# Performance work log

Measured on AMD Instinct MI355X. Metric: run time of the kernel, lower is better.

The kernel has to match this reference:

```python
import jax, jax.numpy as jnp
import numpy as np
from jax import lax

SCALE = 4
PATCH = 3
CR = 2
SOFTMAX_FACTOR = 10.0
B, H, W, C = 8, 64, 64, 64
CI = C // CR


def prelu(x, alpha):
    return jnp.where(x >= 0, x, alpha * x)


def conv1x1(x, w, b):
    return jnp.einsum('bhwc,cd->bhwd', x, w) + b


def _same_pad(in_size, k, s):
    out = -(-in_size // s)
    pad = max((out - 1) * s + k - in_size, 0)
    return pad // 2, pad - pad // 2, out


def extract_patches(x, k, s):
    # x: [B,H,W,C] -> [B, outH, outW, k, k, C], SAME zero padding (TF extract_patches)
    b, h, w, c = x.shape
    plh, phh, oh = _same_pad(h, k, s)
    plw, phw, ow = _same_pad(w, k, s)
    xp = jnp.pad(x, ((0, 0), (plh, phh), (plw, phw), (0, 0)))
    rows = (jnp.arange(oh) * s)[:, None] + jnp.arange(k)[None, :]  # [oh,k]
    cols = (jnp.arange(ow) * s)[:, None] + jnp.arange(k)[None, :]  # [ow,k]
    p = xp[:, rows]              # [B, oh, k, Wp, C]
    p = p[:, :, :, cols]         # [B, oh, k, ow, k, C]
    return p.transpose(0, 1, 3, 2, 4, 5)


def setup_inputs() -> dict:
    key = jax.random.key(0)
    ks = jax.random.split(key, 8)
    def glorot(k, shape):
        fan_in, fan_out = shape[0], shape[1]
        std = np.sqrt(2.0 / (fan_in + fan_out))
        return jax.random.normal(k, shape, dtype=jnp.float32) * std
    return {
        'x': jax.random.normal(ks[0], (B, H, W, C), dtype=jnp.float32),
        'theta_w': glorot(ks[1], (C, CI)),
        'theta_b': jnp.zeros((CI,), jnp.float32),
        'theta_alpha': jax.random.uniform(ks[2], (CI,), jnp.float32, 0.0, 0.3),
        'phi_w': glorot(ks[3], (C, CI)),
        'phi_b': jnp.zeros((CI,), jnp.float32),
        'phi_alpha': jax.random.uniform(ks[4], (CI,), jnp.float32, 0.0, 0.3),
        'g_w': glorot(ks[5], (C, C)),
        'g_b': jnp.zeros((C,), jnp.float32),
        'g_alpha': jax.random.uniform(ks[6], (C,), jnp.float32, 0.0, 0.3),
    }


def reference(x, theta_w, theta_b, theta_alpha, phi_w, phi_b, phi_alpha, g_w, g_b, g_alpha):
    b, h, w, c = x.shape
    s, p = SCALE, PATCH
    hs, ws = h // s, w // s
    n = hs * ws
    sp = s * p
    ci = c // CR

    theta = prelu(conv1x1(x, theta_w, theta_b), theta_alpha)                  # [B,H,W,Ci]
    phi_in = jax.image.resize(x, (b, hs, ws, c), method='bilinear', antialias=False)
    phi = prelu(conv1x1(phi_in, phi_w, phi_b), phi_alpha)                     # [B,Hs,Ws,Ci]
    phi_patch = extract_patches(phi, p, 1).reshape(b, n, p, p, ci)            # [B,N,3,3,Ci]
    g = prelu(conv1x1(x, g_w, g_b), g_alpha)                                  # [B,H,W,C]
    g_patch = extract_patches(g, sp, s).reshape(b, n, sp, sp, c)              # [B,N,12,12,C]

    # L2-normalize each phi patch (per patch, over kh,kw,ci)
    norm = jnp.sqrt(jnp.sum(phi_patch * phi_patch, axis=(2, 3, 4), keepdims=True))
    phi_n = phi_patch / jnp.maximum(norm, 1e-6)

    # patch matching == SAME 3x3 correlation of theta with N dynamic filters
    theta_patch = extract_patches(theta, p, 1)                                # [B,H,W,3,3,Ci]
    scores = jnp.einsum('bhwpqc,bnpqc->bhwn', theta_patch, phi_n)             # [B,H,W,N]
    attn = jax.nn.softmax(scores * SOFTMAX_FACTOR, axis=-1)

    # conv2d_transpose with per-sample filters [sp,sp,C,N], stride s, SAME
    pad_lo, pad_hi, _ = _same_pad(s * h, sp, s)  # forward-conv SAME pads (4,4)
    pads = (sp - 1 - pad_lo, sp - 1 - pad_hi)

    def deconv(y_i, g_i):
        # y_i: [H,W,N]; g_i: [N,sp,sp,C]
        ker = g_i.transpose(1, 2, 0, 3)[::-1, ::-1]  # spatially flipped, HWIO (I=N,O=C)
        out = lax.conv_general_dilated(
            y_i[None], ker, window_strides=(1, 1),
            padding=[pads, pads], lhs_dilation=(s, s),
            dimension_numbers=('NHWC', 'HWIO', 'NHWC'))
        return out[0]

    y = jax.vmap(deconv)(attn, g_patch)  # [B, s*H, s*W, C]
    return y / 6.0
```

## Files before the change

### kernel.cpp

```cpp
#include <hip/hip_runtime.h>
#include <math.h>

#define BB 8

typedef __attribute__((ext_vector_type(8))) short short8;
typedef __attribute__((ext_vector_type(4))) float f32x4;

__device__ inline short f2bf(float x) {
  unsigned u = __builtin_bit_cast(unsigned, x);
  u += 0x7fffu + ((u >> 16) & 1u);
  return (short)(u >> 16);
}
__device__ inline float bf2f(short h) {
  unsigned u = ((unsigned)(unsigned short)h) << 16;
  return __builtin_bit_cast(float, u);
}

__device__ inline void gload_lds16(const void* g, void* l) {
  __builtin_amdgcn_global_load_lds(
      (const __attribute__((address_space(1))) void*)g,
      (__attribute__((address_space(3))) void*)l, 16, 0, 0);
}

__device__ inline void ring_px(int p, int& r, int& cc) {
  if (p < 66) { r = 0; cc = p; }
  else if (p < 132) { r = 65; cc = p - 66; }
  else { int q = p - 132; r = 1 + (q >> 1); cc = (q & 1) ? 65 : 0; }
}

__global__ __launch_bounds__(256) void k_pre(const float* __restrict__ x,
                          const float* __restrict__ theta_w, const float* __restrict__ theta_b,
                          const float* __restrict__ theta_alpha,
                          const float* __restrict__ phi_w, const float* __restrict__ phi_b,
                          const float* __restrict__ phi_alpha,
                          const float* __restrict__ g_w, const float* __restrict__ g_b,
                          const float* __restrict__ g_alpha,
                          short* __restrict__ thetaPh, short* __restrict__ thetaPl,
                          short* __restrict__ gOut,
                          short* __restrict__ Bh, short* __restrict__ Bl) {
  __shared__ __align__(16) float spool[14528];
  int tid = threadIdx.x;
  if (blockIdx.x < 256) {
    int bid = blockIdx.x;
    int b = bid >> 5, pg = bid & 31;
    int px0 = pg * 128;
    if (tid <= 32) {
      int c = pg + 32 * tid;
      if (c < 1040) {
        int p = c >> 2, off = (c & 3) * 8;
        int r, cc; ring_px(p, r, cc);
        size_t ad = ((size_t)(b * 66 + r) * 66 + cc) * 32 + off;
        short8 z = (short8)0;
        *(short8*)(thetaPh + ad) = z;
        *(short8*)(thetaPl + ad) = z;
      }
    }
    float* gw = spool;
    float* tw = spool + 4096;
    float* xs = spool + 6144;
    float* gb_s = spool + 14336; float* ga_s = spool + 14400;
    float* tb_s = spool + 14464; float* ta_s = spool + 14496;
    for (int idx = tid; idx < 1024; idx += 256) ((float4*)gw)[idx] = ((const float4*)g_w)[idx];
    for (int idx = tid; idx < 512; idx += 256)  ((float4*)tw)[idx] = ((const float4*)theta_w)[idx];
    if (tid < 64) { gb_s[tid] = g_b[tid]; ga_s[tid] = g_alpha[tid]; }
    else if (tid < 96) { tb_s[tid - 64] = theta_b[tid - 64]; ta_s[tid - 64] = theta_alpha[tid - 64]; }
    {
      int p = tid >> 1, half = tid & 1;
      const float* xp = x + ((size_t)b * 4096 + px0 + p) * 64 + half * 32;
      #pragma unroll
      for (int i = 0; i < 8; ++i) {
        float4 v = ((const float4*)xp)[i];
        int k = half * 32 + i * 4;
        xs[(k + 0) * 128 + p] = v.x; xs[(k + 1) * 128 + p] = v.y;
        xs[(k + 2) * 128 + p] = v.z; xs[(k + 3) * 128 + p] = v.w;
      }
    }
    __syncthreads();
    int pp = tid >> 2, q = tid & 3;
    float accg[2][16], acct[2][8];
    #pragma unroll
    for (int c = 0; c < 16; ++c) { float bv = gb_s[q * 16 + c]; accg[0][c] = bv; accg[1][c] = bv; }
    #pragma unroll
    for (int c = 0; c < 8; ++c)  { float bv = tb_s[q * 8 + c];  acct[0][c] = bv; acct[1][c] = bv; }
    for (int k = 0; k < 64; ++k) {
      float x0 = xs[k * 128 + 2 * pp], x1 = xs[k * 128 + 2 * pp + 1];
      const float* gwr = gw + k * 64 + q * 16;
      const float* twr = tw + k * 32 + q * 8;
      #pragma unroll
      for (int c = 0; c < 16; ++c) { float wv = gwr[c]; accg[0][c] += x0 * wv; accg[1][c] += x1 * wv; }
      #pragma unroll
      for (int c = 0; c < 8; ++c)  { float wv = twr[c]; acct[0][c] += x0 * wv; acct[1][c] += x1 * wv; }
    }
    #pragma unroll
    for (int e = 0; e < 2; ++e) {
      int px = px0 + 2 * pp + e;
      short* gp = gOut + ((size_t)(b * 4096 + px)) * 64 + q * 16;
      short8 gv0, gv1;
      #pragma unroll
      for (int c = 0; c < 16; ++c) {
        float v = accg[e][c];
        float a = ga_s[q * 16 + c];
        v = v >= 0.f ? v : a * v;
        short hb = f2bf(v);
        if (c < 8) gv0[c] = hb; else gv1[c - 8] = hb;
      }
      *(short8*)(gp) = gv0;
      *(short8*)(gp + 8) = gv1;
      int h = px >> 6, w = px & 63;
      size_t off = ((size_t)(b * 66 + h + 1) * 66 + (w + 1)) * 32 + q * 8;
      short8 hv, lv;
      #pragma unroll
      for (int c = 0; c < 8; ++c) {
        float t = acct[e][c];
        float a = ta_s[q * 8 + c];
        float v = t >= 0.f ? t : a * t;
        short hi = f2bf(v);
        hv[c] = hi;
        lv[c] = f2bf(v - bf2f(hi));
      }
      *(short8*)(thetaPh + off) = hv;
      *(short8*)(thetaPl + off) = lv;
    }
  } else {
    int bid = blockIdx.x - 256;
    int b = bid >> 4, irow = bid & 15;
    float* pw   = spool;
    float* pb   = spool + 2048;
    float* pa   = spool + 2080;
    float* ph_s = spool + 2112;
    float* ss2  = spool + 3696;
    float* ssp  = spool + 3744;
    for (int idx = tid; idx < 512; idx += 256) ((float4*)pw)[idx] = ((const float4*)phi_w)[idx];
    if (tid < 32) { pb[tid] = phi_b[tid]; pa[tid] = phi_alpha[tid]; }
    __syncthreads();
    if (tid < 192) {
      int lr = tid >> 6, j = (tid >> 2) & 15, cg = tid & 3;
      int i2 = irow + lr - 1;
      float acc8[8];
      float sum2 = 0.f;
      if (i2 >= 0 && i2 < 16) {
        #pragma unroll
        for (int c = 0; c < 8; ++c) acc8[c] = pb[cg * 8 + c];
        const float* xb = x + (size_t)b * 4096 * 64;
        const float* p00 = xb + ((size_t)(4 * i2 + 1) * 64 + (4 * j + 1)) * 64;
        for (int kq = 0; kq < 16; ++kq) {
          float4 a = ((const float4*)p00)[kq];
          float4 bq = ((const float4*)(p00 + 64))[kq];
          float4 cq = ((const float4*)(p00 + 4096))[kq];
          float4 dq = ((const float4*)(p00 + 4160))[kq];
          float xv[4] = {0.25f * (a.x + bq.x + cq.x + dq.x), 0.25f * (a.y + bq.y + cq.y + dq.y),
                         0.25f * (a.z + bq.z + cq.z + dq.z), 0.25f * (a.w + bq.w + cq.w + dq.w)};
          #pragma unroll
          for (int e = 0; e < 4; ++e) {
            const float* pwr = pw + (kq * 4 + e) * 32 + cg * 8;
            #pragma unroll
            for (int c = 0; c < 8; ++c) acc8[c] += xv[e] * pwr[c];
          }
        }
        #pragma unroll
        for (int c = 0; c < 8; ++c) {
          float v = acc8[c];
          v = v >= 0.f ? v : pa[cg * 8 + c] * v;
          ph_s[(lr * 16 + j) * 33 + cg * 8 + c] = v;
          sum2 += v * v;
        }
      } else {
        #pragma unroll
        for (int c = 0; c < 8; ++c) ph_s[(lr * 16 + j) * 33 + cg * 8 + c] = 0.f;
      }
      ssp[tid] = sum2;
    }
    __syncthreads();
    if (tid < 48) ss2[tid] = ssp[tid*4] + ssp[tid*4+1] + ssp[tid*4+2] + ssp[tid*4+3];
    __syncthreads();
    int j = tid >> 4, u = tid & 15;
    if (u < 9) {
      float nn = 0.f;
      #pragma unroll
      for (int lr = 0; lr < 3; ++lr) {
        int i2 = irow + lr - 1;
        if (i2 < 0 || i2 > 15) continue;
        #pragma unroll
        for (int dj = 0; dj < 3; ++dj) {
          int pj = j + dj - 1;
          if (pj >= 0 && pj < 16) nn += ss2[lr * 16 + pj];
        }
      }
      float scale = 1.f / fmaxf(sqrtf(nn), 1e-6f);
      int lr = u / 3, dj = u % 3;
      int i2 = irow + lr - 1, pj = j + dj - 1;
      bool ok = (i2 >= 0 && i2 < 16 && pj >= 0 && pj < 16);
      size_t base = ((size_t)(b * 256 + irow * 16 + j)) * 288 + u * 32;
      #pragma unroll
      for (int q8 = 0; q8 < 4; ++q8) {
        short8 hv, lv;
        #pragma unroll
        for (int c = 0; c < 8; ++c) {
          float v = ok ? ph_s[(lr * 16 + pj) * 33 + q8 * 8 + c] * scale : 0.f;
          short hi = f2bf(v);
          hv[c] = hi;
          lv[c] = f2bf(v - bf2f(hi));
        }
        *(short8*)(Bh + base + q8 * 8) = hv;
        *(short8*)(Bl + base + q8 * 8) = lv;
      }
    }
  }
}

__global__ __launch_bounds__(256) void k_bgather(const short* __restrict__ g,
                                                 short* __restrict__ Bbf) {
  int r = blockIdx.x;
  int bl = blockIdx.y;
  int ry = r >> 2, rx = r & 3;
  int t = threadIdx.x;
  int wv = t >> 6, l = t & 63;
  int jj = t >> 4, c4 = (t & 15) * 4;
  __shared__ short tile[256 * 66];
  const short* gb = g + (size_t)bl * 4096 * 64;
  for (int s = 0; s < 9; ++s) {
    int dy = s / 3, dx = s % 3;
    {
      int col = 4 * jj + rx + 4 * dx - 4;
      #pragma unroll
      for (int i2 = 0; i2 < 16; ++i2) {
        int row = 4 * i2 + ry + 4 * dy - 4;
        short4 v = make_short4(0, 0, 0, 0);
        if (row >= 0 && row < 64 && col >= 0 && col < 64)
          v = *(const short4*)(gb + (((size_t)row << 6) + col) * 64 + c4);
        int ij = i2 * 16 + jj;
        tile[ij * 66 + c4 + 0] = v.x;
        tile[ij * 66 + c4 + 1] = v.y;
        tile[ij * 66 + c4 + 2] = v.z;
        tile[ij * 66 + c4 + 3] = v.w;
      }
    }
    __syncthreads();
    #pragma unroll
    for (int cc = 0; cc < 16; ++cc) {
      int c = cc * 4 + wv;
      int n = r * 64 + c;
      unsigned* dstrow = (unsigned*)(Bbf + ((size_t)bl * 1024 + n) * 2304 + s * 256);
      #pragma unroll
      for (int half = 0; half < 2; ++half) {
        int ij0 = half * 128 + 2 * l;
        unsigned v = (unsigned)(unsigned short)tile[ij0 * 66 + c]
                   | ((unsigned)(unsigned short)tile[(ij0 + 1) * 66 + c] << 16);
        dstrow[half * 64 + l] = v;
      }
    }
    __syncthreads();
  }
}

__global__ __launch_bounds__(512) void k_mid(const short* __restrict__ g,
                                             short* __restrict__ Bbf,
                                             const short* __restrict__ thetaPh,
                                             const short* __restrict__ thetaPl,
                                             const short* __restrict__ Bh,
                                             const short* __restrict__ Bl,
                                             short* __restrict__ attnp,
                                             int doGather) {
  __shared__ __align__(16) short smem[32768];
  int tid = threadIdx.x;
  int b = blockIdx.y;
  if (blockIdx.x < 16) {
    if (!doGather) return;
    int r = blockIdx.x, bl = b;
    int ry = r >> 2, rx = r & 3;
    short* tile = smem;
    const short* gb = g + (size_t)bl * 4096 * 64;
    for (int s = 0; s < 9; ++s) {
      int dy = s / 3, dx = s % 3;
      if (tid < 256) {
        int jj = tid >> 4, c4 = (tid & 15) * 4;
        int col = 4 * jj + rx + 4 * dx - 4;
        #pragma unroll
        for (int i2 = 0; i2 < 16; ++i2) {
          int row = 4 * i2 + ry + 4 * dy - 4;
          short4 v = make_short4(0, 0, 0, 0);
          if (row >= 0 && row < 64 && col >= 0 && col < 64)
            v = *(const short4*)(gb + (((size_t)row << 6) + col) * 64 + c4);
          int ij = i2 * 16 + jj;
          tile[ij * 66 + c4 + 0] = v.x;
          tile[ij * 66 + c4 + 1] = v.y;
          tile[ij * 66 + c4 + 2] = v.z;
          tile[ij * 66 + c4 + 3] = v.w;
        }
      }
      __syncthreads();
      if (tid < 256) {
        int wv = tid >> 6, l = tid & 63;
        #pragma unroll
        for (int cc = 0; cc < 16; ++cc) {
          int c = cc * 4 + wv;
          int n = r * 64 + c;
          unsigned* dstrow = (unsigned*)(Bbf + ((size_t)bl * 1024 + n) * 2304 + s * 256);
          #pragma unroll
          for (int half = 0; half < 2; ++half) {
            int ij0 = half * 128 + 2 * l;
            unsigned v = (unsigned)(unsigned short)tile[ij0 * 66 + c]
                       | ((unsigned)(unsigned short)tile[(ij0 + 1) * 66 + c] << 16);
            dstrow[half * 64 + l] = v;
          }
        }
      }
      __syncthreads();
    }
    return;
  }
  int mt = blockIdx.x - 16;
  {
    int c = mt + 32 * tid;
    if (c < 8320) {
      int p = c >> 5, off = (c & 31) * 8;
      int r, cc; ring_px(p, r, cc);
      *(short8*)(attnp + ((size_t)(b * 66 + r) * 66 + cc) * 256 + off) = (short8)0;
    }
  }
  int w = tid >> 6, lane = tid & 63;
  int wm = w >> 2, wn = w & 3;
  int quad = lane >> 4, l16 = lane & 15;

  short* Ash = smem;
  short* Asl = smem + 4096;
  short* Bsh = smem + 8192;
  short* Bsl = smem + 16384;
  float* wred = (float*)(smem + 24576);

  f32x4 acc[4][4];
  #pragma unroll
  for (int i = 0; i < 4; ++i)
    #pragma unroll
    for (int j = 0; j < 4; ++j) acc[i][j] = (f32x4)0.f;

  int ar = w * 16 + (lane >> 2);
  int am = mt * 128 + ar;
  int aQy = am >> 6, aQx = am & 63;
  int achunk = (lane & 3) * 8;

  for (int s = 0; s < 9; ++s) {
    int di = s / 3, dj = s % 3;
    __syncthreads();
    size_t aoff = ((size_t)(b * 66 + aQy + di) * 66 + (aQx + dj)) * 32 + achunk;
    gload_lds16(thetaPh + aoff, Ash + w * 512 + lane * 8);
    gload_lds16(thetaPl + aoff, Asl + w * 512 + lane * 8);
    #pragma unroll
    for (int p = 0; p < 2; ++p) {
      int nl = w * 32 + p * 16 + (lane >> 2);
      size_t boff = ((size_t)(b * 256 + nl)) * 288 + s * 32 + achunk;
      gload_lds16(Bh + boff, Bsh + w * 1024 + p * 512 + lane * 8);
      gload_lds16(Bl + boff, Bsl + w * 1024 + p * 512 + lane * 8);
    }
    __syncthreads();
    #pragma unroll
    for (int pass = 0; pass < 3; ++pass) {
      const short* Asrc = (pass < 2) ? Ash : Asl;
      const short* Bsrc = (pass == 1) ? Bsl : Bsh;
      short8 af[4], bfr[4];
      #pragma unroll
      for (int i = 0; i < 4; ++i)
        af[i] = *(const short8*)(Asrc + (wm * 64 + i * 16 + l16) * 32 + quad * 8);
      #pragma unroll
      for (int j = 0; j < 4; ++j)
        bfr[j] = *(const short8*)(Bsrc + (wn * 64 + j * 16 + l16) * 32 + quad * 8);
      #pragma unroll
      for (int i = 0; i < 4; ++i)
        #pragma unroll
        for (int j = 0; j < 4; ++j)
          acc[i][j] = __builtin_amdgcn_mfma_f32_16x16x32_bf16(af[i], bfr[j], acc[i][j], 0, 0, 0);
    }
  }

  float rmax[4][4];
  #pragma unroll
  for (int i = 0; i < 4; ++i)
    #pragma unroll
    for (int reg = 0; reg < 4; ++reg) {
      float m = -1e30f;
      #pragma unroll
      for (int j = 0; j < 4; ++j) m = fmaxf(m, acc[i][j][reg]);
      #pragma unroll
      for (int off = 1; off < 16; off <<= 1) m = fmaxf(m, __shfl_xor(m, off));
      rmax[i][reg] = m;
    }
  if (l16 == 0) {
    #pragma unroll
    for (int i = 0; i < 4; ++i)
      #pragma unroll
      for (int reg = 0; reg < 4; ++reg)
        wred[(wm * 64 + i * 16 + quad * 4 + reg) * 4 + wn] = rmax[i][reg];
  }
  __syncthreads();
  #pragma unroll
  for (int i = 0; i < 4; ++i)
    #pragma unroll
    for (int reg = 0; reg < 4; ++reg) {
      int r = wm * 64 + i * 16 + quad * 4 + reg;
      rmax[i][reg] = fmaxf(fmaxf(wred[r * 4 + 0], wred[r * 4 + 1]),
                           fmaxf(wred[r * 4 + 2], wred[r * 4 + 3]));
    }
  __syncthreads();
  float rsum[4][4];
  #pragma unroll
  for (int i = 0; i < 4; ++i)
    #pragma unroll
    for (int reg = 0; reg < 4; ++reg) {
      float s = 0.f;
      #pragma unroll
      for (int j = 0; j < 4; ++j) {
        float e = expf((acc[i][j][reg] - rmax[i][reg]) * 10.f);
        acc[i][j][reg] = e;
        s += e;
      }
      #pragma unroll
      for (int off = 1; off < 16; off <<= 1) s += __shfl_xor(s, off);
      rsum[i][reg] = s;
    }
  if (l16 == 0) {
    #pragma unroll
    for (int i = 0; i < 4; ++i)
      #pragma unroll
      for (int reg = 0; reg < 4; ++reg)
        wred[(wm * 64 + i * 16 + quad * 4 + reg) * 4 + wn] = rsum[i][reg];
  }
  __syncthreads();
  #pragma unroll
  for (int i = 0; i < 4; ++i)
    #pragma unroll
    for (int reg = 0; reg < 4; ++reg) {
      int r = wm * 64 + i * 16 + quad * 4 + reg;
      float tot = wred[r * 4 + 0] + wred[r * 4 + 1] + wred[r * 4 + 2] + wred[r * 4 + 3];
      rsum[i][reg] = 1.f / tot;
    }
  __syncthreads();
  #pragma unroll
  for (int i = 0; i < 4; ++i)
    #pragma unroll
    for (int reg = 0; reg < 4; ++reg) {
      int r = wm * 64 + i * 16 + quad * 4 + reg;
      #pragma unroll
      for (int j = 0; j < 4; ++j)
        smem[r * 256 + wn * 64 + j * 16 + l16] = f2bf(acc[i][j][reg] * rsum[i][reg]);
    }
  __syncthreads();
  {
    int r2 = tid >> 2, c2 = (tid & 3) * 64;
    int m2 = mt * 128 + r2;
    int Qy = m2 >> 6, Qx = m2 & 63;
    short8* dst = (short8*)(attnp + ((size_t)(b * 66 + Qy + 1) * 66 + (Qx + 1)) * 256 + c2);
    #pragma unroll
    for (int q = 0; q < 8; ++q) dst[q] = *(const short8*)(smem + r2 * 256 + c2 + q * 8);
  }
}

__global__ __launch_bounds__(256) void k_gemm(const short* __restrict__ attnp,
                                              const short* __restrict__ Bbf,
                                              float* __restrict__ out,
                                              int b0) {
  int lid = blockIdx.x + 32 * blockIdx.y + 256 * blockIdx.z;
  int nwg = 256 * gridDim.z;
  int chunk = nwg >> 3;
  int swz = (lid & 7) * chunk + (lid >> 3);
  int mt = swz & 31;
  int nt = (swz >> 5) & 7;
  int bl = swz >> 8;
  int b = b0 + bl;
  int tid = threadIdx.x;
  int wave = tid >> 6, lane = tid & 63;
  int wm = wave >> 1, wn = wave & 1;
  int quad = lane >> 4, l16 = lane & 15;

  __shared__ __align__(16) short As[8192];
  __shared__ __align__(16) short Bs[8192];

  f32x4 acc[4][4];
  #pragma unroll
  for (int i = 0; i < 4; ++i)
    #pragma unroll
    for (int j = 0; j < 4; ++j) acc[i][j] = (f32x4)0.f;

  const short* Ab = attnp + (size_t)b * 66 * 66 * 256;
  const short* Bb = Bbf + (size_t)bl * 1024 * 2304 + (size_t)(nt * 128) * 2304;

  int larow = lane >> 2;
  int lakq8 = (lane & 3) * 8;

  for (int kb0 = 0; kb0 < 36; ++kb0) {
    __syncthreads();
    #pragma unroll
    for (int u = 0; u < 2; ++u) {
      int kb = kb0 * 2 + u;
      int s = kb >> 3;
      int dy = s / 3, dx = s % 3;
      int n0 = (kb & 7) * 32;
      #pragma unroll
      for (int t = 0; t < 2; ++t) {
        int rr = wave * 32 + t * 16 + larow;
        int m = mt * 128 + rr;
        int hh = (m >> 6) + 2 - dy;
        int wwp = (m & 63) + 2 - dx;
        gload_lds16(Ab + ((size_t)(hh * 66 + wwp) << 8) + n0 + lakq8,
                    As + u * 4096 + wave * 1024 + t * 512 + lane * 8);
        gload_lds16(Bb + (size_t)rr * 2304 + kb * 32 + lakq8,
                    Bs + u * 4096 + wave * 1024 + t * 512 + lane * 8);
      }
    }
    __syncthreads();
    #pragma unroll
    for (int u = 0; u < 2; ++u) {
      short8 af[4], bfr[4];
      #pragma unroll
      for (int i = 0; i < 4; ++i)
        af[i] = *(const short8*)(As + u * 4096 + (wm * 64 + i * 16 + l16) * 32 + quad * 8);
      #pragma unroll
      for (int j = 0; j < 4; ++j)
        bfr[j] = *(const short8*)(Bs + u * 4096 + (wn * 64 + j * 16 + l16) * 32 + quad * 8);
      #pragma unroll
      for (int i = 0; i < 4; ++i)
        #pragma unroll
        for (int j = 0; j < 4; ++j)
          acc[i][j] = __builtin_amdgcn_mfma_f32_16x16x32_bf16(af[i], bfr[j], acc[i][j], 0, 0, 0);
    }
  }

  const float inv6 = 1.f / 6.f;
  #pragma unroll
  for (int i = 0; i < 4; ++i) {
    int mbase = mt * 128 + wm * 64 + i * 16 + quad * 4;
    #pragma unroll
    for (int j = 0; j < 4; ++j) {
      int n = nt * 128 + wn * 64 + j * 16 + l16;
      int r = n >> 6; int c = n & 63;
      int ry = r >> 2, rx = r & 3;
      #pragma unroll
      for (int reg = 0; reg < 4; ++reg) {
        int m = mbase + reg;
        int Qy = m >> 6, Qx = m & 63;
        out[(((size_t)b * 256 + 4 * Qy + ry) * 256 + (4 * Qx + rx)) * 64 + c]
            = acc[i][j][reg] * inv6;
      }
    }
  }
}

extern "C" void kernel_launch(void* const* d_in, const int* in_sizes, int n_in,
                              void* d_out, int out_size, void* d_ws, size_t ws_size,
                              hipStream_t stream) {
  const float* x           = (const float*)d_in[0];
  const float* theta_w     = (const float*)d_in[1];
  const float* theta_b     = (const float*)d_in[2];
  const float* theta_alpha = (const float*)d_in[3];
  const float* phi_w       = (const float*)d_in[4];
  const float* phi_b       = (const float*)d_in[5];
  const float* phi_alpha   = (const float*)d_in[6];
  const float* g_w         = (const float*)d_in[7];
  const float* g_b         = (const float*)d_in[8];
  const float* g_alpha     = (const float*)d_in[9];
  float* out = (float*)d_out;

  char* w = (char*)d_ws;
  size_t off = 0;
  auto alloc = [&](size_t bytes) { void* p = w + off; off += (bytes + 255) & ~255ull; return p; };
  short* g       = (short*)alloc(8ull * 4096 * 64 * 2);
  size_t thp_bytes = 8ull * 66 * 66 * 32 * 2;
  short* thetaPh = (short*)alloc(thp_bytes);
  short* thetaPl = (short*)alloc(thp_bytes);
  short* Bh      = (short*)alloc(8ull * 256 * 288 * 2);
  short* Bl      = (short*)alloc(8ull * 256 * 288 * 2);
  size_t attnp_bytes = 8ull * 66 * 66 * 256 * 2;
  short* attnp   = (short*)alloc(attnp_bytes);
  size_t bbf_full = 8ull * 1024 * 2304 * 2;
  bool full = (off + bbf_full) <= ws_size;
  short* Bbf = (short*)alloc(full ? bbf_full : bbf_full / 8);

  hipLaunchKernelGGL(k_pre, dim3(256 + 128), dim3(256), 0, stream,
                     x, theta_w, theta_b, theta_alpha, phi_w, phi_b, phi_alpha,
                     g_w, g_b, g_alpha, thetaPh, thetaPl, g, Bh, Bl);
  if (full) {
    hipLaunchKernelGGL(k_mid, dim3(48, BB), dim3(512), 0, stream,
                       g, Bbf, thetaPh, thetaPl, Bh, Bl, attnp, 1);
    hipLaunchKernelGGL(k_gemm, dim3(32, 8, BB), dim3(256), 0, stream, attnp, Bbf, out, 0);
  } else {
    hipLaunchKernelGGL(k_mid, dim3(48, BB), dim3(512), 0, stream,
                       g, Bbf, thetaPh, thetaPl, Bh, Bl, attnp, 0);
    for (int b = 0; b < BB; ++b) {
      hipLaunchKernelGGL(k_bgather, dim3(16, 1), dim3(256), 0, stream,
                         g + (size_t)b * 4096 * 64, Bbf);
      hipLaunchKernelGGL(k_gemm, dim3(32, 8, 1), dim3(256), 0, stream, attnp, Bbf, out, b);
    }
  }
}
```

Measured before the change: 384.6 us.

## Double-buffer LDS tiles in deconv GEMM with XOR-swizzled layout

Converts the single-buffered GEMM main loop to a double-buffered prefetch pipeline. The next K tile is loaded into the alternate LDS buffer via global_load_lds while MFMAs run on the current one, with explicit vmcnt waits and barriers. The LDS tile is reorganized to 64-wide rows with an XOR swizzle on the column chunk to reduce bank conflicts on the fragment reads. This doubles LDS use to 64KB per block, which may lower occupancy.

```diff
diff --git a/kernel.cpp b/kernel.cpp
--- a/kernel.cpp
+++ b/kernel.cpp
@@ -471,8 +471,8 @@
   int wm = wave >> 1, wn = wave & 1;
   int quad = lane >> 4, l16 = lane & 15;
 
-  __shared__ __align__(16) short As[8192];
-  __shared__ __align__(16) short Bs[8192];
+  __shared__ __align__(16) short As[2][8192];
+  __shared__ __align__(16) short Bs[2][8192];
 
   f32x4 acc[4][4];
   #pragma unroll
@@ -483,46 +483,62 @@
   const short* Ab = attnp + (size_t)b * 66 * 66 * 256;
   const short* Bb = Bbf + (size_t)bl * 1024 * 2304 + (size_t)(nt * 128) * 2304;
 
-  int larow = lane >> 2;
-  int lakq8 = (lane & 3) * 8;
-
-  for (int kb0 = 0; kb0 < 36; ++kb0) {
-    __syncthreads();
-    #pragma unroll
-    for (int u = 0; u < 2; ++u) {
-      int kb = kb0 * 2 + u;
-      int s = kb >> 3;
-      int dy = s / 3, dx = s % 3;
-      int n0 = (kb & 7) * 32;
-      #pragma unroll
-      for (int t = 0; t < 2; ++t) {
-        int rr = wave * 32 + t * 16 + larow;
-        int m = mt * 128 + rr;
-        int hh = (m >> 6) + 2 - dy;
-        int wwp = (m & 63) + 2 - dx;
-        gload_lds16(Ab + ((size_t)(hh * 66 + wwp) << 8) + n0 + lakq8,
-                    As + u * 4096 + wave * 1024 + t * 512 + lane * 8);
-        gload_lds16(Bb + (size_t)rr * 2304 + kb * 32 + lakq8,
-                    Bs + u * 4096 + wave * 1024 + t * 512 + lane * 8);
-      }
-    }
-    __syncthreads();
-    #pragma unroll
-    for (int u = 0; u < 2; ++u) {
+  int srow = wave * 8 + (lane >> 3);
+  int cl8  = ((lane & 7) ^ (lane >> 3)) * 8;
+  int dsto = tid * 8;
+
+  #define STAGE(kt, buf)                                                        \
+    {                                                                           \
+      int s_ = (kt) >> 2;                                                       \
+      int dy_ = s_ / 3, dx_ = s_ % 3;                                           \
+      int n0_ = ((kt) & 3) * 64 + cl8;                                          \
+      int kc_ = (kt) * 64 + cl8;                                                \
+      _Pragma("unroll")                                                         \
+      for (int r_ = 0; r_ < 4; ++r_) {                                          \
+        int row_ = r_ * 32 + srow;                                              \
+        int m_ = mt * 128 + row_;                                               \
+        int hh_ = (m_ >> 6) + 2 - dy_;                                          \
+        int ww_ = (m_ & 63) + 2 - dx_;                                          \
+        gload_lds16(Ab + ((size_t)(hh_ * 66 + ww_) << 8) + n0_,                 \
+                    &As[buf][r_ * 2048 + dsto]);                                \
+        gload_lds16(Bb + (size_t)row_ * 2304 + kc_,                             \
+                    &Bs[buf][r_ * 2048 + dsto]);                                \
+      }                                                                         \
+    }
+
+  STAGE(0, 0);
+  int pc0 = (quad ^ (l16 & 7)) * 8;
+
+  for (int t = 0; t < 36; ++t) {
+    int cur = t & 1;
+    if (t + 1 < 36) {
+      STAGE(t + 1, cur ^ 1);
+      asm volatile("s_waitcnt vmcnt(8)" ::: "memory");
+    } else {
+      asm volatile("s_waitcnt vmcnt(0)" ::: "memory");
+    }
+    __builtin_amdgcn_s_barrier();
+    __builtin_amdgcn_sched_barrier(0);
+    #pragma unroll
+    for (int ks = 0; ks < 2; ++ks) {
+      int po = pc0 ^ (ks * 32);
       short8 af[4], bfr[4];
       #pragma unroll
       for (int i = 0; i < 4; ++i)
-        af[i] = *(const short8*)(As + u * 4096 + (wm * 64 + i * 16 + l16) * 32 + quad * 8);
+        af[i] = *(const short8*)(&As[cur][(wm * 64 + i * 16 + l16) * 64 + po]);
       #pragma unroll
       for (int j = 0; j < 4; ++j)
-        bfr[j] = *(const short8*)(Bs + u * 4096 + (wn * 64 + j * 16 + l16) * 32 + quad * 8);
+        bfr[j] = *(const short8*)(&Bs[cur][(wn * 64 + j * 16 + l16) * 64 + po]);
       #pragma unroll
       for (int i = 0; i < 4; ++i)
         #pragma unroll
         for (int j = 0; j < 4; ++j)
           acc[i][j] = __builtin_amdgcn_mfma_f32_16x16x32_bf16(af[i], bfr[j], acc[i][j], 0, 0, 0);
     }
-  }
+    __builtin_amdgcn_sched_barrier(0);
+    __builtin_amdgcn_s_barrier();
+  }
+  #undef STAGE
 
   const float inv6 = 1.f / 6.f;
   #pragma unroll
```

Result: no change. 384.9 us (+0.1%).
